# Kernel tuning notes

Hardware: AMD Instinct MI355X
Metric: run time of the kernel (lower is better)

Reference implementation:

```python
import jax, jax.numpy as jnp
import numpy as np

HEAD_DIM = 64
N_HEADS = 16
D_MODEL = 2048
SEQ = 2048
BATCH = 1
LAYER_IDX = 12
LN_EPS = 1e-5


def setup_inputs() -> dict:
    key = jax.random.key(0)
    ks = jax.random.split(key, 8)
    s = 0.02
    return {
        "x": jax.random.normal(ks[0], (BATCH, SEQ, D_MODEL), dtype=jnp.float32),
        "W_qkv": jax.random.normal(ks[1], (3 * N_HEADS * 2 * HEAD_DIM, D_MODEL), dtype=jnp.float32) * s,
        "W_o": jax.random.normal(ks[2], (D_MODEL, D_MODEL), dtype=jnp.float32) * s,
        "lambda_q1": jax.random.normal(ks[3], (2 * HEAD_DIM,), dtype=jnp.float32) * 0.1,
        "lambda_k1": jax.random.normal(ks[4], (2 * HEAD_DIM,), dtype=jnp.float32) * 0.1,
        "lambda_q2": jax.random.normal(ks[5], (2 * HEAD_DIM,), dtype=jnp.float32) * 0.1,
        "lambda_k2": jax.random.normal(ks[6], (2 * HEAD_DIM,), dtype=jnp.float32) * 0.1,
        "gn_gamma": jnp.ones((N_HEADS, 2 * HEAD_DIM), dtype=jnp.float32),
        "gn_beta": jnp.zeros((N_HEADS, 2 * HEAD_DIM), dtype=jnp.float32),
    }


def _causal_sdpa(q, k, v, scale):
    # q,k: [B,H,S,d], v: [B,H,S,2d]
    S = q.shape[2]
    scores = jnp.einsum("bhqd,bhkd->bhqk", q, k) * scale
    causal = jnp.tril(jnp.ones((S, S), dtype=bool))
    scores = jnp.where(causal[None, None], scores, jnp.float32(-1e30))
    attn = jax.nn.softmax(scores, axis=-1)
    return jnp.einsum("bhqk,bhkd->bhqd", attn, v)


def reference(x, W_qkv, W_o, lambda_q1, lambda_k1, lambda_q2, lambda_k2, gn_gamma, gn_beta):
    B, S, D = x.shape
    lambda_init = 0.8 - 0.6 * jnp.exp(jnp.float32(-0.3 * LAYER_IDX))
    scale = HEAD_DIM ** -0.5

    qkv = x @ W_qkv.T  # [B,S,6*H*d]
    qkv = qkv.reshape(B, S, 3, N_HEADS, 2 * HEAD_DIM)
    q = jnp.transpose(qkv[:, :, 0], (0, 2, 1, 3))  # [B,H,S,2d]
    k = jnp.transpose(qkv[:, :, 1], (0, 2, 1, 3))
    v = jnp.transpose(qkv[:, :, 2], (0, 2, 1, 3))
    q1, q2 = q[..., :HEAD_DIM], q[..., HEAD_DIM:]
    k1, k2 = k[..., :HEAD_DIM], k[..., HEAD_DIM:]

    lam = jnp.exp(lambda_q1 * lambda_k1) - jnp.exp(lambda_q2 * lambda_k2) + lambda_init  # [2d]

    A1 = _causal_sdpa(q1, k1, v, scale)
    A2 = _causal_sdpa(q2, k2, v, scale)
    out = A1 - lam * A2  # broadcast over value channel [B,H,S,2d]

    # per-head LayerNorm over last dim
    mu = jnp.mean(out, axis=-1, keepdims=True)
    var = jnp.mean((out - mu) ** 2, axis=-1, keepdims=True)
    out = (out - mu) * jax.lax.rsqrt(var + LN_EPS)
    out = out * gn_gamma[None, :, None, :] + gn_beta[None, :, None, :]

    out = out * (1.0 - lambda_init)
    out = jnp.transpose(out, (0, 2, 1, 3)).reshape(B, S, D)
    return out @ W_o.T
```

## Files before the change

kernel.cpp:

```cpp
#include <hip/hip_runtime.h>

typedef short short8 __attribute__((ext_vector_type(8)));
typedef float f32x4 __attribute__((ext_vector_type(4)));
typedef unsigned short u16;
typedef u16 u16x8 __attribute__((ext_vector_type(8)));
typedef u16 u16x4 __attribute__((ext_vector_type(4)));

__device__ static inline u16 f2bf(float f) {
    union { float f; unsigned u; } v; v.f = f;
    unsigned r = v.u + 0x7fffu + ((v.u >> 16) & 1u);
    return (u16)(r >> 16);
}

__device__ static inline unsigned cvt_pk_bf16(float a, float b) {
    unsigned r;
    asm("v_cvt_pk_bf16_f32 %0, %1, %2" : "=v"(r) : "v"(a), "v"(b));
    return r;
}

__global__ __launch_bounds__(256) void cast3_kernel(const float* __restrict__ xa,
                                                    u16* __restrict__ xo,
                                                    const float* __restrict__ wa,
                                                    u16* __restrict__ wo,
                                                    const float* __restrict__ oa,
                                                    u16* __restrict__ oo) {
    const int bid = blockIdx.x;
    const float* in;
    u16* out;
    int b;
    if (bid < 4096)        { in = xa; out = xo; b = bid; }
    else if (bid < 16384)  { in = wa; out = wo; b = bid - 4096; }
    else                   { in = oa; out = oo; b = bid - 16384; }
    int i = (b * 256 + threadIdx.x) * 4;
    f32x4 v = *(const f32x4*)&in[i];
    union { unsigned w[2]; u16x4 s; } o;
    o.w[0] = cvt_pk_bf16(v[0], v[1]);
    o.w[1] = cvt_pk_bf16(v[2], v[3]);
    *(u16x4*)&out[i] = o.s;
}

template <int BM, int BN, int MODE, int MINW>
__global__ __launch_bounds__(256, MINW) void gemm_bt(const u16* __restrict__ A,
                                                     const u16* __restrict__ B,
                                                     int M, int N, int K,
                                                     float* __restrict__ C,
                                                     u16* __restrict__ Qo,
                                                     u16* __restrict__ Ko,
                                                     u16* __restrict__ Vo) {
    constexpr int APT = BM * 4 / 256;
    constexpr int BPT = BN * 4 / 256;
    constexpr int MT = BM / 32, NT = BN / 32;
    __shared__ u16 As[BM * 32];
    __shared__ u16 Bs[BN * 32];
    const int tid  = threadIdx.x;
    const int lane = tid & 63, wave = tid >> 6;
    const int quad = lane >> 4, l15 = lane & 15;
    const int wm = wave >> 1, wn = wave & 1;
    const int m0 = blockIdx.y * BM;
    const int n0 = blockIdx.x * BN;

    f32x4 acc[MT][NT] = {};

    const u16* aga[APT];
    const u16* bga[BPT];
#pragma unroll
    for (int i = 0; i < APT; i++) {
        int s = tid + i * 256, r = s >> 2;
        int kg = (s & 3) ^ ((r >> 1) & 3);
        aga[i] = &A[(size_t)(m0 + r) * K + kg * 8];
    }
#pragma unroll
    for (int i = 0; i < BPT; i++) {
        int s = tid + i * 256, r = s >> 2;
        int kg = (s & 3) ^ ((r >> 1) & 3);
        bga[i] = &B[(size_t)(n0 + r) * K + kg * 8];
    }

    u16x8 ast[APT], bst[BPT];
#pragma unroll
    for (int i = 0; i < APT; i++) ast[i] = *(const u16x8*)aga[i];
#pragma unroll
    for (int i = 0; i < BPT; i++) bst[i] = *(const u16x8*)bga[i];

    for (int k0 = 0; k0 < K; k0 += 32) {
        if (k0) __syncthreads();
#pragma unroll
        for (int i = 0; i < APT; i++) *(u16x8*)&As[(tid + i * 256) * 8] = ast[i];
#pragma unroll
        for (int i = 0; i < BPT; i++) *(u16x8*)&Bs[(tid + i * 256) * 8] = bst[i];
        __syncthreads();
        if (k0 + 32 < K) {
#pragma unroll
            for (int i = 0; i < APT; i++) ast[i] = *(const u16x8*)(aga[i] + k0 + 32);
#pragma unroll
            for (int i = 0; i < BPT; i++) bst[i] = *(const u16x8*)(bga[i] + k0 + 32);
        }

        short8 af[MT], bf[NT];
#pragma unroll
        for (int mt = 0; mt < MT; mt++) {
            int row = wm * (BM / 2) + mt * 16 + l15;
            int slot = row * 4 + (quad ^ ((row >> 1) & 3));
            af[mt] = *(const short8*)&As[slot * 8];
        }
#pragma unroll
        for (int nt = 0; nt < NT; nt++) {
            int row = wn * (BN / 2) + nt * 16 + l15;
            int slot = row * 4 + (quad ^ ((row >> 1) & 3));
            bf[nt] = *(const short8*)&Bs[slot * 8];
        }
#pragma unroll
        for (int mt = 0; mt < MT; mt++)
#pragma unroll
            for (int nt = 0; nt < NT; nt++)
                acc[mt][nt] = __builtin_amdgcn_mfma_f32_16x16x32_bf16(af[mt], bf[nt], acc[mt][nt], 0, 0, 0);
    }

    if (MODE == 0) {
#pragma unroll
        for (int mt = 0; mt < MT; mt++)
#pragma unroll
            for (int nt = 0; nt < NT; nt++)
#pragma unroll
                for (int r = 0; r < 4; r++) {
                    int row = m0 + wm * (BM / 2) + mt * 16 + quad * 4 + r;
                    int col = n0 + wn * (BN / 2) + nt * 16 + l15;
                    C[(size_t)row * N + col] = acc[mt][nt][r];
                }
    } else {
        const int comp = n0 >> 11, h = (n0 >> 7) & 15;
        u16* dst = (comp == 0) ? Qo : ((comp == 1) ? Ko : Vo);
        const float sc = (comp == 0) ? 0.18033688f : 1.0f;
#pragma unroll
        for (int mt = 0; mt < MT; mt++)
#pragma unroll
            for (int nt = 0; nt < NT; nt++)
#pragma unroll
                for (int r = 0; r < 4; r++) {
                    int row = m0 + wm * (BM / 2) + mt * 16 + quad * 4 + r;
                    int d = wn * (BN / 2) + nt * 16 + l15;
                    dst[((h * 2048) + row) * 128 + d] = f2bf(acc[mt][nt][r] * sc);
                }
    }
}

__global__ __launch_bounds__(256) void transpose_v(const u16* __restrict__ vb,
                                                   u16* __restrict__ vT) {
    __shared__ u16 T[64 * 136];
    const int s0 = blockIdx.x * 64, h = blockIdx.y;
    const int tid = threadIdx.x;
#pragma unroll
    for (int i = 0; i < 4; i++) {
        int c = tid + i * 256;
        int s = c >> 4, dch = c & 15;
        *(u16x8*)&T[s * 136 + dch * 8] =
            *(const u16x8*)&vb[((h * 2048) + s0 + s) * 128 + dch * 8];
    }
    __syncthreads();
#pragma unroll
    for (int i = 0; i < 4; i++) {
        int c = tid + i * 256;
        int d = c >> 3, sch = c & 7;
        u16x8 o;
#pragma unroll
        for (int j = 0; j < 8; j++) o[j] = T[(sch * 8 + j) * 136 + d];
        *(u16x8*)&vT[((h * 128) + d) * 2048 + s0 + sch * 8] = o;
    }
}

__global__ __launch_bounds__(256, 2) void attn_kernel(const u16* __restrict__ qb,
                                                      const u16* __restrict__ kb,
                                                      const u16* __restrict__ vT,
                                                      float* __restrict__ ob) {
    const int bid = blockIdx.x;
    const int h = bid & 15;
    const int comp = (bid >> 4) & 1;
    const int j = bid >> 5;
    const int J = (j < 8) ? (2 * j + 1) : (30 - 2 * j);
    const int nkt = 2 * J + 2;
    const int q0 = J * 128;
    const int tid = threadIdx.x, lane = tid & 63, wave = tid >> 6;
    const int quad = lane >> 4, l15 = lane & 15;
    const int qh = quad >> 1, ql = quad & 1;

    __shared__ u16 Ks[64 * 64];
    __shared__ u16 VsT[128 * 64];
    const char* KsB = (const char*)Ks;
    const char* VsB = (const char*)VsT;

    const u16* kb_h = &kb[(size_t)h * 2048 * 128 + comp * 64];
    const u16* vT_h = &vT[(size_t)h * 128 * 2048];

    const int c1 = tid, c2 = tid + 256;
    const int k1key = c1 >> 3, k1dc = ((c1 & 7) ^ k1key) & 7;
    const int k2key = c2 >> 3, k2dc = ((c2 & 7) ^ k2key) & 7;
    const u16* kaddr1 = &kb_h[k1key * 128 + k1dc * 8];
    const u16* kaddr2 = &kb_h[k2key * 128 + k2dc * 8];
    const u16* vaddr[4];
#pragma unroll
    for (int i = 0; i < 4; i++) {
        int c = tid + i * 256;
        int dim = c >> 3, kc = ((c & 7) ^ dim) & 7;
        vaddr[i] = &vT_h[dim * 2048 + kc * 8];
    }

    const int koff0 = l15 * 128 + ((quad ^ l15) & 7) * 16;
    const int koff1 = l15 * 128 + (((quad + 4) ^ l15) & 7) * 16;
    int vb[8][2];
#pragma unroll
    for (int nt = 0; nt < 8; nt++) {
        int dim = nt * 16 + l15;
        int base = dim * 128 + ((qh ^ dim) & 7) * 16 + ql * 8;
        vb[nt][0] = base;
        vb[nt][1] = base ^ 64;
    }

    short8 aq[2][2];
#pragma unroll
    for (int qs = 0; qs < 2; qs++)
#pragma unroll
        for (int ks = 0; ks < 2; ks++) {
            int qrow = q0 + wave * 32 + qs * 16 + l15;
            aq[qs][ks] = *(const short8*)
                &qb[((h * 2048) + qrow) * 128 + comp * 64 + ks * 32 + quad * 8];
        }

    float l_acc[2] = {0.f, 0.f};
    f32x4 acc[8][2] = {};

    u16x8 kst0, kst1, vst[4];
    kst0 = *(const u16x8*)kaddr1;
    kst1 = *(const u16x8*)kaddr2;
#pragma unroll
    for (int i = 0; i < 4; i++) vst[i] = *(const u16x8*)vaddr[i];
    const u16* kp1 = kaddr1 + 8192;
    const u16* kp2 = kaddr2 + 8192;
    const u16* vp[4];
#pragma unroll
    for (int i = 0; i < 4; i++) vp[i] = vaddr[i] + 64;

    for (int kt = 0; kt < nkt; kt++) {
        *(u16x8*)&Ks[c1 * 8] = kst0;
        *(u16x8*)&Ks[c2 * 8] = kst1;
#pragma unroll
        for (int i = 0; i < 4; i++) *(u16x8*)&VsT[(tid + i * 256) * 8] = vst[i];
        __syncthreads();

        if (kt + 1 < nkt) {
            kst0 = *(const u16x8*)kp1; kp1 += 8192;
            kst1 = *(const u16x8*)kp2; kp2 += 8192;
#pragma unroll
            for (int i = 0; i < 4; i++) { vst[i] = *(const u16x8*)vp[i]; vp[i] += 64; }
        }

        short8 kf[4][2];
#pragma unroll
        for (int kn = 0; kn < 4; kn++) {
            kf[kn][0] = *(const short8*)(KsB + (koff0 + kn * 2048));
            kf[kn][1] = *(const short8*)(KsB + (koff1 + kn * 2048));
        }

        short8 b8[2][2];
#pragma unroll
        for (int qs = 0; qs < 2; qs++) {
#pragma unroll
            for (int kn2 = 0; kn2 < 2; kn2++) {
                f32x4 sa = {}, sb = {};
                sa = __builtin_amdgcn_mfma_f32_16x16x32_bf16(kf[2 * kn2][0], aq[qs][0], sa, 0, 0, 0);
                sa = __builtin_amdgcn_mfma_f32_16x16x32_bf16(kf[2 * kn2][1], aq[qs][1], sa, 0, 0, 0);
                sb = __builtin_amdgcn_mfma_f32_16x16x32_bf16(kf[2 * kn2 + 1][0], aq[qs][0], sb, 0, 0, 0);
                sb = __builtin_amdgcn_mfma_f32_16x16x32_bf16(kf[2 * kn2 + 1][1], aq[qs][1], sb, 0, 0, 0);
                if (kt >= nkt - 2) {
                    int q = q0 + wave * 32 + qs * 16 + l15;
                    int kb0 = kt * 64 + kn2 * 32 + quad * 4;
#pragma unroll
                    for (int r = 0; r < 4; r++) {
                        if (kb0 + r > q) sa[r] = -1e30f;
                        if (kb0 + 16 + r > q) sb[r] = -1e30f;
                    }
                }
                float p0 = exp2f(sa[0]), p1 = exp2f(sa[1]), p2 = exp2f(sa[2]), p3 = exp2f(sa[3]);
                float p4 = exp2f(sb[0]), p5 = exp2f(sb[1]), p6 = exp2f(sb[2]), p7 = exp2f(sb[3]);
                l_acc[qs] += ((p0 + p1) + (p2 + p3)) + ((p4 + p5) + (p6 + p7));
                union { unsigned w[4]; short8 s; } pw;
                pw.w[0] = cvt_pk_bf16(p0, p1);
                pw.w[1] = cvt_pk_bf16(p2, p3);
                pw.w[2] = cvt_pk_bf16(p4, p5);
                pw.w[3] = cvt_pk_bf16(p6, p7);
                b8[qs][kn2] = pw.s;
            }
        }

        __builtin_amdgcn_s_setprio(1);
#pragma unroll
        for (int nt = 0; nt < 8; nt++) {
#pragma unroll
            for (int kn2 = 0; kn2 < 2; kn2++) {
                union { u16x4 h4[2]; short8 s; } av;
                int o0 = vb[nt][kn2];
                av.h4[0] = *(const u16x4*)(VsB + o0);
                av.h4[1] = *(const u16x4*)(VsB + (o0 ^ 32));
                acc[nt][0] = __builtin_amdgcn_mfma_f32_16x16x32_bf16(av.s, b8[0][kn2], acc[nt][0], 0, 0, 0);
                acc[nt][1] = __builtin_amdgcn_mfma_f32_16x16x32_bf16(av.s, b8[1][kn2], acc[nt][1], 0, 0, 0);
            }
        }
        __builtin_amdgcn_s_setprio(0);
        __syncthreads();
    }

#pragma unroll
    for (int qs = 0; qs < 2; qs++) {
        l_acc[qs] += __shfl_xor(l_acc[qs], 16);
        l_acc[qs] += __shfl_xor(l_acc[qs], 32);
    }
    float rl[2] = {1.f / l_acc[0], 1.f / l_acc[1]};

#pragma unroll
    for (int qs = 0; qs < 2; qs++) {
        int s = q0 + wave * 32 + qs * 16 + l15;
        float* orow = &ob[((size_t)(comp * 16 + h) * 2048 + s) * 128 + quad * 4];
#pragma unroll
        for (int nt = 0; nt < 8; nt++) {
            f32x4 v;
#pragma unroll
            for (int r = 0; r < 4; r++) v[r] = acc[nt][qs][r] * rl[qs];
            *(f32x4*)&orow[nt * 16] = v;
        }
    }
}

__global__ __launch_bounds__(256) void combine_kernel(const float* __restrict__ ob,
                                                      const float* __restrict__ lq1,
                                                      const float* __restrict__ lk1,
                                                      const float* __restrict__ lq2,
                                                      const float* __restrict__ lk2,
                                                      const float* __restrict__ gamma,
                                                      const float* __restrict__ beta,
                                                      u16* __restrict__ attn) {
    const int tid = threadIdx.x, wave = tid >> 6, lane = tid & 63;
    const int row = blockIdx.x * 4 + wave;
    const int s = row >> 4, h = row & 15;
    const float lambda_init = 0.8f - 0.6f * __expf(-3.6f);
    const int d0 = lane * 2;
    float vals[2];
#pragma unroll
    for (int j = 0; j < 2; j++) {
        int d = d0 + j;
        float a1 = ob[((h)*2048 + s) * 128 + d];
        float a2 = ob[((16 + h) * 2048 + s) * 128 + d];
        float lam = __expf(lq1[d] * lk1[d]) - __expf(lq2[d] * lk2[d]) + lambda_init;
        vals[j] = a1 - lam * a2;
    }
    float sum = vals[0] + vals[1];
    float sq = vals[0] * vals[0] + vals[1] * vals[1];
#pragma unroll
    for (int off = 1; off < 64; off <<= 1) {
        sum += __shfl_xor(sum, off);
        sq += __shfl_xor(sq, off);
    }
    float mu = sum * (1.f / 128.f);
    float var = sq * (1.f / 128.f) - mu * mu;
    float rinv = rsqrtf(var + 1e-5f);
    float osc = 1.f - lambda_init;
#pragma unroll
    for (int j = 0; j < 2; j++) {
        int d = d0 + j;
        float g = gamma[h * 128 + d], b = beta[h * 128 + d];
        float v = ((vals[j] - mu) * rinv * g + b) * osc;
        attn[s * 2048 + h * 128 + d] = f2bf(v);
    }
}

extern "C" void kernel_launch(void* const* d_in, const int* in_sizes, int n_in,
                              void* d_out, int out_size, void* d_ws, size_t ws_size,
                              hipStream_t stream) {
    (void)in_sizes; (void)n_in; (void)out_size; (void)ws_size;
    const float* x    = (const float*)d_in[0];
    const float* Wqkv = (const float*)d_in[1];
    const float* Wo   = (const float*)d_in[2];
    const float* lq1  = (const float*)d_in[3];
    const float* lk1  = (const float*)d_in[4];
    const float* lq2  = (const float*)d_in[5];
    const float* lk2  = (const float*)d_in[6];
    const float* gam  = (const float*)d_in[7];
    const float* bet  = (const float*)d_in[8];
    float* out = (float*)d_out;

    char* ws = (char*)d_ws;
    u16*   xb    = (u16*)(ws);
    u16*   wqkvb = (u16*)(ws + (size_t)(8 << 20));
    float* ob    = (float*)(ws + (size_t)(8 << 20));
    u16*   wob   = (u16*)(ws + (size_t)(40 << 20));
    u16*   qb    = (u16*)(ws + (size_t)(48 << 20));
    u16*   kb    = (u16*)(ws + (size_t)(56 << 20));
    u16*   vb    = (u16*)(ws + (size_t)(64 << 20));
    u16*   vT    = (u16*)(ws + (size_t)(72 << 20));
    u16*   attn  = (u16*)(ws);

    cast3_kernel<<<20480, 256, 0, stream>>>(x, xb, Wqkv, wqkvb, Wo, wob);
    gemm_bt<128, 128, 1, 3><<<dim3(48, 16), 256, 0, stream>>>(
        xb, wqkvb, 2048, 6144, 2048, nullptr, qb, kb, vb);
    transpose_v<<<dim3(32, 16), 256, 0, stream>>>(vb, vT);
    attn_kernel<<<512, 256, 0, stream>>>(qb, kb, vT, ob);
    combine_kernel<<<8192, 256, 0, stream>>>(ob, lq1, lk1, lq2, lk2, gam, bet, attn);
    gemm_bt<128, 64, 0, 2><<<dim3(32, 16), 256, 0, stream>>>(
        attn, wob, 2048, 2048, 2048, out, nullptr, nullptr, nullptr);
}
```

Before: 287.2 us.

## Split long causal attention tiles along keys and merge partials in combine

Query tiles in the second half of the sequence, which have the longest key ranges, are split into two key-range halves run by separate blocks. The split blocks write unnormalized partial outputs and row sums, placing the second partial in the output buffer as scratch, and the combine kernel adds the partials and normalizes them. A constant table orders the 768 blocks so long and short work mix for better load balance, and launch bounds are raised to 3 blocks per CU to allow more occupancy. The cost is extra partial-output traffic and register pressure from the higher occupancy target; merging without max-tracking is safe only because the softmax has no running max.

Measured after the change: 358.3 us. 24.8% more time.

```diff
diff --git a/kernel.cpp b/kernel.cpp
--- a/kernel.cpp
+++ b/kernel.cpp
@@ -17,6 +17,11 @@
     asm("v_cvt_pk_bf16_f32 %0, %1, %2" : "=v"(r) : "v"(a), "v"(b));
     return r;
 }
+
+__constant__ unsigned char ATT_MAP[24] = {
+    61, 28, 57, 59, 55, 24, 20, 45,
+    63, 53, 49, 41, 16, 43, 51, 47,
+     0,  4,  8, 12, 37, 33, 39, 35};
 
 __global__ __launch_bounds__(256) void cast3_kernel(const float* __restrict__ xa,
                                                     u16* __restrict__ xo,
@@ -168,16 +173,22 @@
     }
 }
 
-__global__ __launch_bounds__(256, 2) void attn_kernel(const u16* __restrict__ qb,
+__global__ __launch_bounds__(256, 3) void attn_kernel(const u16* __restrict__ qb,
                                                       const u16* __restrict__ kb,
                                                       const u16* __restrict__ vT,
-                                                      float* __restrict__ ob) {
+                                                      float* __restrict__ ob,
+                                                      float* __restrict__ op1,
+                                                      float* __restrict__ lb0,
+                                                      float* __restrict__ lb1) {
     const int bid = blockIdx.x;
     const int h = bid & 15;
     const int comp = (bid >> 4) & 1;
-    const int j = bid >> 5;
-    const int J = (j < 8) ? (2 * j + 1) : (30 - 2 * j);
+    const int u = bid >> 5;
+    const int e = ATT_MAP[u];
+    const int J = e >> 2, half = (e >> 1) & 1, split = e & 1;
     const int nkt = 2 * J + 2;
+    const int kt0 = (split && half) ? (J + 1) : 0;
+    const int kt1 = (split && !half) ? (J + 1) : nkt;
     const int q0 = J * 128;
     const int tid = threadIdx.x, lane = tid & 63, wave = tid >> 6;
     const int quad = lane >> 4, l15 = lane & 15;
@@ -206,13 +217,13 @@
 
     const int koff0 = l15 * 128 + ((quad ^ l15) & 7) * 16;
     const int koff1 = l15 * 128 + (((quad + 4) ^ l15) & 7) * 16;
-    int vb[8][2];
+    int vbo[8][2];
 #pragma unroll
     for (int nt = 0; nt < 8; nt++) {
         int dim = nt * 16 + l15;
         int base = dim * 128 + ((qh ^ dim) & 7) * 16 + ql * 8;
-        vb[nt][0] = base;
-        vb[nt][1] = base ^ 64;
+        vbo[nt][0] = base;
+        vbo[nt][1] = base ^ 64;
     }
 
     short8 aq[2][2];
@@ -229,24 +240,24 @@
     f32x4 acc[8][2] = {};
 
     u16x8 kst0, kst1, vst[4];
-    kst0 = *(const u16x8*)kaddr1;
-    kst1 = *(const u16x8*)kaddr2;
-#pragma unroll
-    for (int i = 0; i < 4; i++) vst[i] = *(const u16x8*)vaddr[i];
-    const u16* kp1 = kaddr1 + 8192;
-    const u16* kp2 = kaddr2 + 8192;
+    kst0 = *(const u16x8*)(kaddr1 + kt0 * 8192);
+    kst1 = *(const u16x8*)(kaddr2 + kt0 * 8192);
+#pragma unroll
+    for (int i = 0; i < 4; i++) vst[i] = *(const u16x8*)(vaddr[i] + kt0 * 64);
+    const u16* kp1 = kaddr1 + (kt0 + 1) * 8192;
+    const u16* kp2 = kaddr2 + (kt0 + 1) * 8192;
     const u16* vp[4];
 #pragma unroll
-    for (int i = 0; i < 4; i++) vp[i] = vaddr[i] + 64;
-
-    for (int kt = 0; kt < nkt; kt++) {
+    for (int i = 0; i < 4; i++) vp[i] = vaddr[i] + (kt0 + 1) * 64;
+
+    for (int kt = kt0; kt < kt1; kt++) {
         *(u16x8*)&Ks[c1 * 8] = kst0;
         *(u16x8*)&Ks[c2 * 8] = kst1;
 #pragma unroll
         for (int i = 0; i < 4; i++) *(u16x8*)&VsT[(tid + i * 256) * 8] = vst[i];
         __syncthreads();
 
-        if (kt + 1 < nkt) {
+        if (kt + 1 < kt1) {
             kst0 = *(const u16x8*)kp1; kp1 += 8192;
             kst1 = *(const u16x8*)kp2; kp2 += 8192;
 #pragma unroll
@@ -297,7 +308,7 @@
 #pragma unroll
             for (int kn2 = 0; kn2 < 2; kn2++) {
                 union { u16x4 h4[2]; short8 s; } av;
-                int o0 = vb[nt][kn2];
+                int o0 = vbo[nt][kn2];
                 av.h4[0] = *(const u16x4*)(VsB + o0);
                 av.h4[1] = *(const u16x4*)(VsB + (o0 ^ 32));
                 acc[nt][0] = __builtin_amdgcn_mfma_f32_16x16x32_bf16(av.s, b8[0][kn2], acc[nt][0], 0, 0, 0);
@@ -313,23 +324,51 @@
         l_acc[qs] += __shfl_xor(l_acc[qs], 16);
         l_acc[qs] += __shfl_xor(l_acc[qs], 32);
     }
-    float rl[2] = {1.f / l_acc[0], 1.f / l_acc[1]};
-
-#pragma unroll
-    for (int qs = 0; qs < 2; qs++) {
-        int s = q0 + wave * 32 + qs * 16 + l15;
-        float* orow = &ob[((size_t)(comp * 16 + h) * 2048 + s) * 128 + quad * 4];
-#pragma unroll
-        for (int nt = 0; nt < 8; nt++) {
-            f32x4 v;
-#pragma unroll
-            for (int r = 0; r < 4; r++) v[r] = acc[nt][qs][r] * rl[qs];
-            *(f32x4*)&orow[nt * 16] = v;
+
+    if (!split) {
+        float rl[2] = {1.f / l_acc[0], 1.f / l_acc[1]};
+#pragma unroll
+        for (int qs = 0; qs < 2; qs++) {
+            int s = q0 + wave * 32 + qs * 16 + l15;
+            float* orow = &ob[((size_t)(comp * 16 + h) * 2048 + s) * 128 + quad * 4];
+#pragma unroll
+            for (int nt = 0; nt < 8; nt++) {
+                f32x4 v;
+#pragma unroll
+                for (int r = 0; r < 4; r++) v[r] = acc[nt][qs][r] * rl[qs];
+                *(f32x4*)&orow[nt * 16] = v;
+            }
+        }
+    } else {
+#pragma unroll
+        for (int qs = 0; qs < 2; qs++) {
+            int s = q0 + wave * 32 + qs * 16 + l15;
+            float* orow = (half == 0)
+                ? &ob[((size_t)(comp * 16 + h) * 2048 + s) * 128 + quad * 4]
+                : &op1[((size_t)(comp * 16 + h) * 1024 + (s - 1024)) * 128 + quad * 4];
+#pragma unroll
+            for (int nt = 0; nt < 8; nt++) {
+                f32x4 v;
+#pragma unroll
+                for (int r = 0; r < 4; r++) v[r] = acc[nt][qs][r];
+                *(f32x4*)&orow[nt * 16] = v;
+            }
+        }
+        float* lbp = ((half == 0) ? lb0 : lb1) + (comp * 16 + h) * 1024;
+        if (quad == 0) {
+#pragma unroll
+            for (int qs = 0; qs < 2; qs++) {
+                int s = q0 + wave * 32 + qs * 16 + l15;
+                lbp[s - 1024] = l_acc[qs];
+            }
         }
     }
 }
 
 __global__ __launch_bounds__(256) void combine_kernel(const float* __restrict__ ob,
+                                                      const float* __restrict__ op1,
+                                                      const float* __restrict__ lb0,
+                                                      const float* __restrict__ lb1,
                                                       const float* __restrict__ lq1,
                                                       const float* __restrict__ lk1,
                                                       const float* __restrict__ lq2,
@@ -342,12 +381,24 @@
     const int s = row >> 4, h = row & 15;
     const float lambda_init = 0.8f - 0.6f * __expf(-3.6f);
     const int d0 = lane * 2;
+    const bool sp = (s >= 1024);
+    float r1 = 1.f, r2 = 1.f;
+    if (sp) {
+        int i1 = h * 1024 + (s - 1024);
+        int i2 = (16 + h) * 1024 + (s - 1024);
+        r1 = 1.f / (lb0[i1] + lb1[i1]);
+        r2 = 1.f / (lb0[i2] + lb1[i2]);
+    }
     float vals[2];
 #pragma unroll
     for (int j = 0; j < 2; j++) {
         int d = d0 + j;
-        float a1 = ob[((h)*2048 + s) * 128 + d];
+        float a1 = ob[((h) * 2048 + s) * 128 + d];
         float a2 = ob[((16 + h) * 2048 + s) * 128 + d];
+        if (sp) {
+            a1 = (a1 + op1[((size_t)h * 1024 + (s - 1024)) * 128 + d]) * r1;
+            a2 = (a2 + op1[((size_t)(16 + h) * 1024 + (s - 1024)) * 128 + d]) * r2;
+        }
         float lam = __expf(lq1[d] * lk1[d]) - __expf(lq2[d] * lk2[d]) + lambda_init;
         vals[j] = a1 - lam * a2;
     }
@@ -396,13 +447,17 @@
     u16*   vb    = (u16*)(ws + (size_t)(64 << 20));
     u16*   vT    = (u16*)(ws + (size_t)(72 << 20));
     u16*   attn  = (u16*)(ws);
+    float* lb0   = (float*)(ws + (size_t)(64 << 20));
+    float* lb1   = (float*)(ws + (size_t)(64 << 20) + (1 << 17));
+    float* op1   = out;
 
     cast3_kernel<<<20480, 256, 0, stream>>>(x, xb, Wqkv, wqkvb, Wo, wob);
     gemm_bt<128, 128, 1, 3><<<dim3(48, 16), 256, 0, stream>>>(
         xb, wqkvb, 2048, 6144, 2048, nullptr, qb, kb, vb);
     transpose_v<<<dim3(32, 16), 256, 0, stream>>>(vb, vT);
-    attn_kernel<<<512, 256, 0, stream>>>(qb, kb, vT, ob);
-    combine_kernel<<<8192, 256, 0, stream>>>(ob, lq1, lk1, lq2, lk2, gam, bet, attn);
+    attn_kernel<<<768, 256, 0, stream>>>(qb, kb, vT, ob, op1, lb0, lb1);
+    combine_kernel<<<8192, 256, 0, stream>>>(ob, op1, lb0, lb1,
+                                             lq1, lk1, lq2, lk2, gam, bet, attn);
     gemm_bt<128, 64, 0, 2><<<dim3(32, 16), 256, 0, stream>>>(
         attn, wob, 2048, 2048, 2048, out, nullptr, nullptr, nullptr);
 }
```

## Replace QKV GEMM with 256x256-tile 8-wave kernel using direct global-to-LDS loads

Applied to the files above, without the earlier changes.

Adds a new QKV projection GEMM that uses 256x256 output tiles per 512-thread block. It streams A and B sub-tiles straight into LDS with global_load_lds, double-buffered and interleaved with the MFMA work of the four quadrants. The goal is more data reuse per tile and overlap of loads with math compared to the old 128x128 tiled GEMM. The cost is higher register and LDS pressure, and the grid shrinks to 192 blocks, which may underfill the GPU's compute units. The epilogue still scatters bf16 values to Q/K/V one element at a time.

Result: faster. 275.7 us (-4.0%).

```diff
diff --git a/kernel.cpp b/kernel.cpp
--- a/kernel.cpp
+++ b/kernel.cpp
@@ -16,6 +16,13 @@
     unsigned r;
     asm("v_cvt_pk_bf16_f32 %0, %1, %2" : "=v"(r) : "v"(a), "v"(b));
     return r;
+}
+
+__device__ static inline void gload16(const u16* g, u16* l) {
+    __builtin_amdgcn_global_load_lds(
+        (const __attribute__((address_space(1))) unsigned int*)g,
+        (__attribute__((address_space(3))) unsigned int*)l,
+        16, 0, 0);
 }
 
 __global__ __launch_bounds__(256) void cast3_kernel(const float* __restrict__ xa,
@@ -39,6 +46,128 @@
     *(u16x4*)&out[i] = o.s;
 }
 
+__global__ __launch_bounds__(512, 2) void gemm_qkv8(const u16* __restrict__ A,
+                                                    const u16* __restrict__ B,
+                                                    u16* __restrict__ Qo,
+                                                    u16* __restrict__ Ko,
+                                                    u16* __restrict__ Vo) {
+    constexpr int K = 2048, NTL = K / 64;
+    __shared__ u16 lds[2][4][128 * 64];
+    const int tid = threadIdx.x;
+    const int lane = tid & 63, wave = tid >> 6;
+    const int quad = lane >> 4, l15 = lane & 15;
+    const int rs = wave >> 1, ch = wave & 1;
+    const int m0 = blockIdx.y * 256, n0 = blockIdx.x * 256;
+
+    const u16* gsrc[4][2];
+#pragma unroll
+    for (int j = 0; j < 2; j++) {
+        int s = j * 512 + tid;
+        int row = s >> 3;
+        int g = (s & 7) ^ (row & 7);
+        gsrc[0][j] = &A[(size_t)(m0 + row) * K + g * 8];
+        gsrc[1][j] = &B[(size_t)(n0 + row) * K + g * 8];
+        gsrc[2][j] = &B[(size_t)(n0 + 128 + row) * K + g * 8];
+        gsrc[3][j] = &A[(size_t)(m0 + 128 + row) * K + g * 8];
+    }
+    const int ldst = wave * 512;
+
+    int offA[2][2], offB[4][2];
+#pragma unroll
+    for (int mf = 0; mf < 2; mf++)
+#pragma unroll
+        for (int ku = 0; ku < 2; ku++) {
+            int lr = rs * 32 + mf * 16 + l15;
+            offA[mf][ku] = lr * 128 + (((ku * 4 + quad) ^ (lr & 7)) * 16);
+        }
+#pragma unroll
+    for (int nf = 0; nf < 4; nf++)
+#pragma unroll
+        for (int ku = 0; ku < 2; ku++) {
+            int lb = ch * 64 + nf * 16 + l15;
+            offB[nf][ku] = lb * 128 + (((ku * 4 + quad) ^ (lb & 7)) * 16);
+        }
+
+    f32x4 acc[2][2][2][4] = {};
+    short8 af[2][2], bf[4][2];
+
+#pragma unroll
+    for (int u = 0; u < 4; u++) {
+        gload16(gsrc[u][0], &lds[0][u][ldst]);
+        gload16(gsrc[u][1], &lds[0][u][ldst + 4096]);
+    }
+
+#define LOAD_A(MH)                                                             \
+    {                                                                          \
+        const char* ub = Lp + (MH ? 3 : 0) * 16384;                            \
+        _Pragma("unroll") for (int mf = 0; mf < 2; mf++)                       \
+            _Pragma("unroll") for (int ku = 0; ku < 2; ku++)                   \
+                af[mf][ku] = *(const short8*)(ub + offA[mf][ku]);              \
+    }
+#define LOAD_B(NH)                                                             \
+    {                                                                          \
+        const char* ub = Lp + (NH ? 2 : 1) * 16384;                            \
+        _Pragma("unroll") for (int nf = 0; nf < 4; nf++)                       \
+            _Pragma("unroll") for (int ku = 0; ku < 2; ku++)                   \
+                bf[nf][ku] = *(const short8*)(ub + offB[nf][ku]);              \
+    }
+#define MMA(MH, NH)                                                            \
+    __builtin_amdgcn_s_setprio(1);                                             \
+    _Pragma("unroll") for (int mf = 0; mf < 2; mf++)                           \
+        _Pragma("unroll") for (int nf = 0; nf < 4; nf++)                       \
+            _Pragma("unroll") for (int ku = 0; ku < 2; ku++)                   \
+                acc[MH][NH][mf][nf] = __builtin_amdgcn_mfma_f32_16x16x32_bf16( \
+                    af[mf][ku], bf[nf][ku], acc[MH][NH][mf][nf], 0, 0, 0);     \
+    __builtin_amdgcn_s_setprio(0);
+#define WAITBAR                                                                \
+    asm volatile("s_waitcnt vmcnt(4)" ::: "memory");                           \
+    __builtin_amdgcn_s_barrier();                                              \
+    asm volatile("" ::: "memory");
+#define STAGE(u)                                                               \
+    gload16(gsrc[u][0] + ko, &lds[pn][u][ldst]);                               \
+    gload16(gsrc[u][1] + ko, &lds[pn][u][ldst + 4096]);
+
+    for (int t = 0; t < NTL; t++) {
+        const int p = t & 1, pn = p ^ 1;
+        const int ko = (t + 1 < NTL) ? (t + 1) * 64 : t * 64;
+        const char* Lp = (const char*)lds[p];
+
+        WAITBAR; STAGE(0);
+        LOAD_A(0); LOAD_B(0); MMA(0, 0);
+        WAITBAR; STAGE(1);
+        LOAD_B(1); MMA(0, 1);
+        WAITBAR; STAGE(2);
+        LOAD_A(1); MMA(1, 1);
+        STAGE(3);
+        LOAD_B(0); MMA(1, 0);
+    }
+#undef LOAD_A
+#undef LOAD_B
+#undef MMA
+#undef WAITBAR
+#undef STAGE
+
+    const int comp = n0 >> 11;
+    u16* dst = (comp == 0) ? Qo : ((comp == 1) ? Ko : Vo);
+    const float sc = (comp == 0) ? 0.18033688f : 1.0f;
+#pragma unroll
+    for (int MH = 0; MH < 2; MH++)
+#pragma unroll
+        for (int NH = 0; NH < 2; NH++)
+#pragma unroll
+            for (int mf = 0; mf < 2; mf++)
+#pragma unroll
+                for (int nf = 0; nf < 4; nf++)
+#pragma unroll
+                    for (int r = 0; r < 4; r++) {
+                        int row = m0 + MH * 128 + rs * 32 + mf * 16 + quad * 4 + r;
+                        int d = (n0 & 2047) + NH * 128 + ch * 64 + nf * 16 + l15;
+                        int h = d >> 7, dd = d & 127;
+                        dst[((h * 2048) + row) * 128 + dd] =
+                            f2bf(acc[MH][NH][mf][nf][r] * sc);
+                    }
+}
+
 template <int BM, int BN, int MODE, int MINW>
 __global__ __launch_bounds__(256, MINW) void gemm_bt(const u16* __restrict__ A,
                                                      const u16* __restrict__ B,
@@ -206,13 +335,13 @@
 
     const int koff0 = l15 * 128 + ((quad ^ l15) & 7) * 16;
     const int koff1 = l15 * 128 + (((quad + 4) ^ l15) & 7) * 16;
-    int vb[8][2];
+    int vbo[8][2];
 #pragma unroll
     for (int nt = 0; nt < 8; nt++) {
         int dim = nt * 16 + l15;
         int base = dim * 128 + ((qh ^ dim) & 7) * 16 + ql * 8;
-        vb[nt][0] = base;
-        vb[nt][1] = base ^ 64;
+        vbo[nt][0] = base;
+        vbo[nt][1] = base ^ 64;
     }
 
     short8 aq[2][2];
@@ -297,7 +426,7 @@
 #pragma unroll
             for (int kn2 = 0; kn2 < 2; kn2++) {
                 union { u16x4 h4[2]; short8 s; } av;
-                int o0 = vb[nt][kn2];
+                int o0 = vbo[nt][kn2];
                 av.h4[0] = *(const u16x4*)(VsB + o0);
                 av.h4[1] = *(const u16x4*)(VsB + (o0 ^ 32));
                 acc[nt][0] = __builtin_amdgcn_mfma_f32_16x16x32_bf16(av.s, b8[0][kn2], acc[nt][0], 0, 0, 0);
@@ -398,8 +527,7 @@
     u16*   attn  = (u16*)(ws);
 
     cast3_kernel<<<20480, 256, 0, stream>>>(x, xb, Wqkv, wqkvb, Wo, wob);
-    gemm_bt<128, 128, 1, 3><<<dim3(48, 16), 256, 0, stream>>>(
-        xb, wqkvb, 2048, 6144, 2048, nullptr, qb, kb, vb);
+    gemm_qkv8<<<dim3(24, 8), 512, 0, stream>>>(xb, wqkvb, qb, kb, vb);
     transpose_v<<<dim3(32, 16), 256, 0, stream>>>(vb, vT);
     attn_kernel<<<512, 256, 0, stream>>>(qb, kb, vT, ob);
     combine_kernel<<<8192, 256, 0, stream>>>(ob, lq1, lk1, lq2, lk2, gam, bet, attn);
```
